# Optimization experiments

Measured on AMD Instinct MI355X. Metric: run time of the kernel, lower is better.

Reference implementation:

```python
import jax, jax.numpy as jnp
import numpy as np

B, N, FE, CIN, COUT, H = 4, 256, 8, 16, 16, 64


def setup_inputs() -> dict:
    key = jax.random.key(0)
    k0, k1, k2, k3, k4 = jax.random.split(key, 5)
    node_attr = jax.random.normal(k0, (B, N, CIN), dtype=jnp.float32)
    edge_adj = jax.random.normal(k1, (B, N, N, FE), dtype=jnp.float32)
    # edge-network MLP: FE -> H (ReLU) -> CIN*COUT
    W1 = jax.random.normal(k2, (FE, H), dtype=jnp.float32) * (1.0 / np.sqrt(FE))
    b1 = jnp.zeros((H,), dtype=jnp.float32)
    W2 = jax.random.normal(k3, (H, CIN * COUT), dtype=jnp.float32) * (1.0 / np.sqrt(H))
    b2 = jnp.zeros((CIN * COUT,), dtype=jnp.float32)
    bound = 1.0 / np.sqrt(CIN)
    root = jax.random.uniform(k4, (CIN, COUT), dtype=jnp.float32, minval=-bound, maxval=bound)
    return {"node_attr": node_attr, "edge_adj": edge_adj, "W1": W1, "b1": b1,
            "W2": W2, "b2": b2, "root": root}


def reference(node_attr, edge_adj, W1, b1, W2, b2, root):
    b, n = edge_adj.shape[0], edge_adj.shape[1]
    cin, cout = root.shape
    fe = edge_adj.shape[-1]
    # net over all N^2 edge features -> per-edge [Cin, Cout] weight matrices
    e = edge_adj.reshape(b, n * n, fe)
    h = jax.nn.relu(e @ W1 + b1)                       # [B, N*N, H]
    w = (h @ W2 + b2).reshape(b, n, n, cin, cout)      # [B, i, j, Cin, Cout]
    # gather index = scatter index = (k mod N): edge (i,j) reads node j,
    # scatter-sums into node j  =>  out[j] = sum_i x[j] @ W[i, j]
    msg = jnp.einsum('bjc,bijcd->bijd', node_attr, w)  # [B, i, j, Cout]
    out = msg.sum(axis=1)                              # [B, N, Cout]
    out = out + node_attr @ root                       # root/self term
    return out
```

## Files before the change

kernel.cpp:

```cpp
#include <hip/hip_runtime.h>

#define B_   4
#define N_   256
#define FE_  8
#define CIN_ 16
#define COUT_ 16
#define H_   64

__global__ __launch_bounds__(256) void nnconv_fused_kernel(
    const float* __restrict__ node_attr,
    const float* __restrict__ edge_adj,
    const float* __restrict__ W1,
    const float* __restrict__ b1,
    const float* __restrict__ W2,
    const float* __restrict__ b2,
    const float* __restrict__ root,
    float* __restrict__ out)
{
    const int bj   = blockIdx.x;
    const int b    = bj >> 8;
    const int j    = bj & (N_ - 1);
    const int t    = threadIdx.x;
    const int lane = t & 63;
    const int wave = t >> 6;

    __shared__ float e_s[N_][FE_];
    __shared__ float hpart[4][H_];
    __shared__ float Hsum[H_];
    __shared__ float contrib[CIN_][COUT_];

    {
        const float4* src = (const float4*)(edge_adj +
            (((size_t)b * N_ + t) * N_ + j) * FE_);
        float4 a0 = src[0];
        float4 a1 = src[1];
        float4* dst = (float4*)(&e_s[t][0]);
        dst[0] = a0;
        dst[1] = a1;
    }

    float w1r[FE_];
    #pragma unroll
    for (int f = 0; f < FE_; ++f) w1r[f] = W1[f * H_ + lane];
    const float b1r = b1[lane];

    __syncthreads();

    float acc = 0.f;
    #pragma unroll 4
    for (int i = wave; i < N_; i += 4) {
        const float4* ev = (const float4*)(&e_s[i][0]);
        float4 e0 = ev[0];
        float4 e1 = ev[1];
        float v = b1r;
        v = fmaf(e0.x, w1r[0], v);
        v = fmaf(e0.y, w1r[1], v);
        v = fmaf(e0.z, w1r[2], v);
        v = fmaf(e0.w, w1r[3], v);
        v = fmaf(e1.x, w1r[4], v);
        v = fmaf(e1.y, w1r[5], v);
        v = fmaf(e1.z, w1r[6], v);
        v = fmaf(e1.w, w1r[7], v);
        acc += fmaxf(v, 0.f);
    }
    hpart[wave][lane] = acc;
    __syncthreads();

    if (t < H_) {
        Hsum[t] = hpart[0][t] + hpart[1][t] + hpart[2][t] + hpart[3][t];
    }
    __syncthreads();

    float ws = (float)N_ * b2[t];
    #pragma unroll 8
    for (int h = 0; h < H_; ++h) {
        ws = fmaf(Hsum[h], W2[h * (CIN_ * COUT_) + t], ws);
    }

    const int c = t >> 4;
    const int d = t & 15;
    const float nodec = node_attr[((size_t)b * N_ + j) * CIN_ + c];
    contrib[c][d] = nodec * (ws + root[t]);
    __syncthreads();

    if (t < COUT_) {
        float o = 0.f;
        #pragma unroll
        for (int cc = 0; cc < CIN_; ++cc) o += contrib[cc][t];
        out[((size_t)b * N_ + j) * COUT_ + t] = o;
    }
}

extern "C" void kernel_launch(void* const* d_in, const int* in_sizes, int n_in,
                              void* d_out, int out_size, void* d_ws, size_t ws_size,
                              hipStream_t stream) {
    const float* node_attr = (const float*)d_in[0];
    const float* edge_adj  = (const float*)d_in[1];
    const float* W1        = (const float*)d_in[2];
    const float* b1        = (const float*)d_in[3];
    const float* W2        = (const float*)d_in[4];
    const float* b2        = (const float*)d_in[5];
    const float* root      = (const float*)d_in[6];
    float* out = (float*)d_out;

    dim3 grid(B_ * N_);
    dim3 block(256);
    nnconv_fused_kernel<<<grid, block, 0, stream>>>(
        node_attr, edge_adj, W1, b1, W2, b2, root, out);
}
```

Measured before the change: 80.68 us.

## Split into coalesced partial hidden-sum kernel and output kernel via workspace

Replaces the single fused kernel, which gathered a strided column of edge features per output node, with two kernels. The first reads edge features in coalesced rows, computes the first MLP layer with ReLU, and accumulates per-(j,h) partial sums in shared memory via atomics, writing them to a workspace. The second kernel reduces the 32 partial slices per node and applies W2, b2, the root term and the node features. This trades strided global reads for an extra launch, shared atomics and about 8 MB of extra workspace traffic.

```diff
diff --git a/kernel.cpp b/kernel.cpp
--- a/kernel.cpp
+++ b/kernel.cpp
@@ -1,74 +1,110 @@
 #include <hip/hip_runtime.h>
 
-#define B_   4
-#define N_   256
-#define FE_  8
-#define CIN_ 16
+#define B_    4
+#define N_    256
+#define FE_   8
+#define CIN_  16
 #define COUT_ 16
-#define H_   64
+#define H_    64
+#define S_    32
 
-__global__ __launch_bounds__(256) void nnconv_fused_kernel(
-    const float* __restrict__ node_attr,
+
+__global__ __launch_bounds__(256) void k1_partial_hsum(
     const float* __restrict__ edge_adj,
     const float* __restrict__ W1,
     const float* __restrict__ b1,
+    float* __restrict__ partial)
+{
+    const int blk = blockIdx.x;
+    const int s   = blk >> 4;
+    const int b   = (blk >> 2) & 3;
+    const int jt  = blk & 3;
+    const int t    = threadIdx.x;
+    const int lane = t & 63;
+    const int w    = t >> 6;
+
+    __shared__ float Hs[H_][65];
+
+    for (int idx = t; idx < H_ * 65; idx += 256) ((float*)Hs)[idx] = 0.f;
+
+    const int i0 = s * 8 + w * 2;
+    const int j  = jt * 64 + lane;
+    const float* e0p = edge_adj + (((size_t)b * N_ + i0)     * N_ + j) * FE_;
+    const float* e1p = edge_adj + (((size_t)b * N_ + i0 + 1) * N_ + j) * FE_;
+    const float4 e0a = ((const float4*)e0p)[0];
+    const float4 e0b = ((const float4*)e0p)[1];
+    const float4 e1a = ((const float4*)e1p)[0];
+    const float4 e1b = ((const float4*)e1p)[1];
+
+    __syncthreads();
+
+    #pragma unroll 4
+    for (int h = 0; h < H_; ++h) {
+        const float w0 = W1[0 * H_ + h];
+        const float w1 = W1[1 * H_ + h];
+        const float w2 = W1[2 * H_ + h];
+        const float w3 = W1[3 * H_ + h];
+        const float w4 = W1[4 * H_ + h];
+        const float w5 = W1[5 * H_ + h];
+        const float w6 = W1[6 * H_ + h];
+        const float w7 = W1[7 * H_ + h];
+        const float bb = b1[h];
+
+        float v0 = bb, v1 = bb;
+        v0 = fmaf(e0a.x, w0, v0);  v1 = fmaf(e1a.x, w0, v1);
+        v0 = fmaf(e0a.y, w1, v0);  v1 = fmaf(e1a.y, w1, v1);
+        v0 = fmaf(e0a.z, w2, v0);  v1 = fmaf(e1a.z, w2, v1);
+        v0 = fmaf(e0a.w, w3, v0);  v1 = fmaf(e1a.w, w3, v1);
+        v0 = fmaf(e0b.x, w4, v0);  v1 = fmaf(e1b.x, w4, v1);
+        v0 = fmaf(e0b.y, w5, v0);  v1 = fmaf(e1b.y, w5, v1);
+        v0 = fmaf(e0b.z, w6, v0);  v1 = fmaf(e1b.z, w6, v1);
+        v0 = fmaf(e0b.w, w7, v0);  v1 = fmaf(e1b.w, w7, v1);
+
+        const float r = fmaxf(v0, 0.f) + fmaxf(v1, 0.f);
+        atomicAdd(&Hs[h][lane], r);
+    }
+    __syncthreads();
+
+    float* dst = partial + (size_t)blk * (64 * 64);
+    #pragma unroll 4
+    for (int k = 0; k < 16; ++k) {
+        const int cell = k * 256 + t;
+        dst[cell] = Hs[cell & 63][cell >> 6];
+    }
+}
+
+__global__ __launch_bounds__(256) void k2_output(
+    const float* __restrict__ node_attr,
     const float* __restrict__ W2,
     const float* __restrict__ b2,
     const float* __restrict__ root,
+    const float* __restrict__ partial,
     float* __restrict__ out)
 {
-    const int bj   = blockIdx.x;
-    const int b    = bj >> 8;
-    const int j    = bj & (N_ - 1);
-    const int t    = threadIdx.x;
-    const int lane = t & 63;
-    const int wave = t >> 6;
+    const int bj = blockIdx.x;
+    const int b  = bj >> 8;
+    const int j  = bj & (N_ - 1);
+    const int jt = j >> 6;
+    const int jj = j & 63;
+    const int t  = threadIdx.x;
 
-    __shared__ float e_s[N_][FE_];
-    __shared__ float hpart[4][H_];
+    __shared__ float sp[4][H_];
     __shared__ float Hsum[H_];
     __shared__ float contrib[CIN_][COUT_];
 
     {
-        const float4* src = (const float4*)(edge_adj +
-            (((size_t)b * N_ + t) * N_ + j) * FE_);
-        float4 a0 = src[0];
-        float4 a1 = src[1];
-        float4* dst = (float4*)(&e_s[t][0]);
-        dst[0] = a0;
-        dst[1] = a1;
+        const int sw = t >> 6;
+        const int h  = t & 63;
+        float a = 0.f;
+        #pragma unroll
+        for (int k = 0; k < 8; ++k) {
+            const int s = sw + k * 4;
+            a += partial[(((size_t)(s * 16 + b * 4 + jt)) * 64 + jj) * 64 + h];
+        }
+        sp[sw][h] = a;
     }
-
-    float w1r[FE_];
-    #pragma unroll
-    for (int f = 0; f < FE_; ++f) w1r[f] = W1[f * H_ + lane];
-    const float b1r = b1[lane];
-
     __syncthreads();
-
-    float acc = 0.f;
-    #pragma unroll 4
-    for (int i = wave; i < N_; i += 4) {
-        const float4* ev = (const float4*)(&e_s[i][0]);
-        float4 e0 = ev[0];
-        float4 e1 = ev[1];
-        float v = b1r;
-        v = fmaf(e0.x, w1r[0], v);
-        v = fmaf(e0.y, w1r[1], v);
-        v = fmaf(e0.z, w1r[2], v);
-        v = fmaf(e0.w, w1r[3], v);
-        v = fmaf(e1.x, w1r[4], v);
-        v = fmaf(e1.y, w1r[5], v);
-        v = fmaf(e1.z, w1r[6], v);
-        v = fmaf(e1.w, w1r[7], v);
-        acc += fmaxf(v, 0.f);
-    }
-    hpart[wave][lane] = acc;
-    __syncthreads();
-
-    if (t < H_) {
-        Hsum[t] = hpart[0][t] + hpart[1][t] + hpart[2][t] + hpart[3][t];
-    }
+    if (t < H_) Hsum[t] = sp[0][t] + sp[1][t] + sp[2][t] + sp[3][t];
     __syncthreads();
 
     float ws = (float)N_ * b2[t];
@@ -103,8 +139,10 @@
     const float* root      = (const float*)d_in[6];
     float* out = (float*)d_out;
 
-    dim3 grid(B_ * N_);
-    dim3 block(256);
-    nnconv_fused_kernel<<<grid, block, 0, stream>>>(
-        node_attr, edge_adj, W1, b1, W2, b2, root, out);
+    float* partial = (float*)d_ws;
+
+    k1_partial_hsum<<<dim3(S_ * B_ * 4), dim3(256), 0, stream>>>(
+        edge_adj, W1, b1, partial);
+    k2_output<<<dim3(B_ * N_), dim3(256), 0, stream>>>(
+        node_attr, W2, b2, root, partial, out);
 }
```

Measured after the change: 120.4 us. +49.2%, slower.
